# Performance work log

Hardware: AMD Instinct MI355X
Metric: run time of the kernel (lower is better)

## Reference

```python
import jax, jax.numpy as jnp
import numpy as np

H = 128

def _lstm_dir(x, w_ih, w_hh, b_ih, b_hh, reverse):
    # x: [B,T,D]; w_ih: [4H,D]; w_hh: [4H,H]; gate order i,f,g,o (PyTorch)
    B = x.shape[0]
    pre = jnp.einsum('btd,gd->btg', x, w_ih) + b_ih + b_hh  # [B,T,4H]
    if reverse:
        pre = pre[:, ::-1]
    pre = jnp.swapaxes(pre, 0, 1)  # [T,B,4H]
    h0 = jnp.zeros((B, H), dtype=x.dtype)
    c0 = jnp.zeros((B, H), dtype=x.dtype)

    def step(carry, xt):
        h, c = carry
        gates = xt + h @ w_hh.T
        i, f, g, o = jnp.split(gates, 4, axis=-1)
        c = jax.nn.sigmoid(f) * c + jax.nn.sigmoid(i) * jnp.tanh(g)
        h = jax.nn.sigmoid(o) * jnp.tanh(c)
        return (h, c), h

    _, hs = jax.lax.scan(step, (h0, c0), pre)  # hs: [T,B,H]
    hs = jnp.swapaxes(hs, 0, 1)  # [B,T,H]
    if reverse:
        hs = hs[:, ::-1]
    return hs

def _bilstm_layer(x, wf, rf):
    fwd = _lstm_dir(x, *wf, reverse=False)
    bwd = _lstm_dir(x, *rf, reverse=True)
    return jnp.concatenate([fwd, bwd], axis=-1)

def setup_inputs() -> dict:
    key = jax.random.key(0)
    ks = jax.random.split(key, 32)
    s = 0.05
    d = {'x': jax.random.normal(ks[0], (64, 512, 64), dtype=jnp.float32)}
    i = 1
    for l, din in [(0, 64), (1, 2 * H)]:
        for suf in ['', 'r']:
            d[f'w_ih_l{l}{suf}'] = s * jax.random.normal(ks[i], (4 * H, din)); i += 1
            d[f'w_hh_l{l}{suf}'] = s * jax.random.normal(ks[i], (4 * H, H)); i += 1
            d[f'b_ih_l{l}{suf}'] = s * jax.random.normal(ks[i], (4 * H,)); i += 1
            d[f'b_hh_l{l}{suf}'] = s * jax.random.normal(ks[i], (4 * H,)); i += 1
    d['w_fc'] = s * jax.random.normal(ks[i], (64, 2 * H)); i += 1
    d['b_fc'] = s * jax.random.normal(ks[i], (64,))
    return d

def reference(x, w_ih_l0, w_hh_l0, b_ih_l0, b_hh_l0, w_ih_l0r, w_hh_l0r, b_ih_l0r, b_hh_l0r, w_ih_l1, w_hh_l1, b_ih_l1, b_hh_l1, w_ih_l1r, w_hh_l1r, b_ih_l1r, b_hh_l1r, w_fc, b_fc):
    h = _bilstm_layer(x, (w_ih_l0, w_hh_l0, b_ih_l0, b_hh_l0), (w_ih_l0r, w_hh_l0r, b_ih_l0r, b_hh_l0r))
    h = _bilstm_layer(h, (w_ih_l1, w_hh_l1, b_ih_l1, b_hh_l1), (w_ih_l1r, w_hh_l1r, b_ih_l1r, b_hh_l1r))
    return h @ w_fc.T + b_fc
```

## Files before the change

### kernel.cpp

```cpp
#include <hip/hip_runtime.h>

#define TT 512
#define BB 64
#define HH 128
#define G4 512
#define PF 4

typedef float f32x4  __attribute__((ext_vector_type(4)));
typedef _Float16 f16x4v __attribute__((ext_vector_type(4)));
typedef _Float16 f16x8v __attribute__((ext_vector_type(8)));

__device__ __forceinline__ void barrier_lds_only() {
    asm volatile("s_waitcnt lgkmcnt(0)\n\ts_barrier" ::: "memory");
}

__global__ __launch_bounds__(256) void convert_f16(
    const float4* __restrict__ src, f16x4v* __restrict__ dst, int n4)
{
    for (int i = blockIdx.x * 256 + threadIdx.x; i < n4; i += gridDim.x * 256) {
        float4 f = src[i];
        f16x4v h;
        h[0] = (_Float16)f.x; h[1] = (_Float16)f.y;
        h[2] = (_Float16)f.z; h[3] = (_Float16)f.w;
        dst[i] = h;
    }
}

template<int K>
__global__ __launch_bounds__(256) void gemm_f16(
    const _Float16* __restrict__ Af, const _Float16* __restrict__ Wf,
    const float* __restrict__ b0, const float* __restrict__ b1,
    float* __restrict__ C)
{
    constexpr int NC  = K / 32;
    constexpr int LDA = 40;
    __shared__ _Float16 As[128 * LDA];
    __shared__ _Float16 Ws[128 * LDA];

    const int bm  = blockIdx.x * 128;
    const int bn  = blockIdx.y * 128;
    const int tid = threadIdx.x;
    const int wv  = tid >> 6;
    const int l   = tid & 63;
    const int jl  = l & 15;
    const int rg  = l >> 4;
    const int wr  = wv >> 1;
    const int wc  = wv & 1;

    const int sr = tid >> 1;
    const int sc = (tid & 1) * 16;

    const _Float16* Ap = Af + (size_t)(bm + sr) * K + sc;
    const _Float16* Wp = Wf + (size_t)(bn + sr) * K + sc;

    f32x4 acc[4][4];
    #pragma unroll
    for (int i = 0; i < 4; ++i)
        #pragma unroll
        for (int j = 0; j < 4; ++j)
            acc[i][j] = (f32x4){0.f, 0.f, 0.f, 0.f};

    f16x8v pa[2], pw[2];
    pa[0] = *(const f16x8v*)(Ap);     pa[1] = *(const f16x8v*)(Ap + 8);
    pw[0] = *(const f16x8v*)(Wp);     pw[1] = *(const f16x8v*)(Wp + 8);

    #pragma unroll 1
    for (int c = 0; c < NC; ++c) {
        __syncthreads();
        {
            int off = sr * LDA + sc;
            *(f16x8v*)&As[off]     = pa[0];
            *(f16x8v*)&As[off + 8] = pa[1];
            *(f16x8v*)&Ws[off]     = pw[0];
            *(f16x8v*)&Ws[off + 8] = pw[1];
        }
        __syncthreads();
        if (c + 1 < NC) {
            pa[0] = *(const f16x8v*)(Ap + (c + 1) * 32);
            pa[1] = *(const f16x8v*)(Ap + (c + 1) * 32 + 8);
            pw[0] = *(const f16x8v*)(Wp + (c + 1) * 32);
            pw[1] = *(const f16x8v*)(Wp + (c + 1) * 32 + 8);
        }
        f16x8v ah[4], wh[4];
        #pragma unroll
        for (int t = 0; t < 4; ++t) {
            ah[t] = *(const f16x8v*)&As[(wr * 64 + t * 16 + jl) * LDA + rg * 8];
            wh[t] = *(const f16x8v*)&Ws[(wc * 64 + t * 16 + jl) * LDA + rg * 8];
        }
        #pragma unroll
        for (int tm = 0; tm < 4; ++tm)
            #pragma unroll
            for (int tn = 0; tn < 4; ++tn)
                acc[tm][tn] = __builtin_amdgcn_mfma_f32_16x16x32_f16(
                    ah[tm], wh[tn], acc[tm][tn], 0, 0, 0);
    }

    #pragma unroll
    for (int tn = 0; tn < 4; ++tn) {
        int n = bn + wc * 64 + tn * 16 + jl;
        float bias = b0[n] + b1[n];
        #pragma unroll
        for (int tm = 0; tm < 4; ++tm) {
            int m = bm + wr * 64 + tm * 16 + rg * 4;
            #pragma unroll
            for (int r = 0; r < 4; ++r)
                C[(size_t)(m + r) * G4 + n] = acc[tm][tn][r] + bias;
        }
    }
}

__global__ __launch_bounds__(512) void lstm_scan_v14(
    const float* __restrict__ pre_f, const float* __restrict__ pre_b,
    const float* __restrict__ whh_f, const float* __restrict__ whh_b,
    float* __restrict__ out)
{
    const int dir = blockIdx.x >> 6;
    const int b   = blockIdx.x & 63;
    const float* __restrict__ pre  = dir ? pre_b : pre_f;
    const float* __restrict__ w_hh = dir ? whh_b : whh_f;

    const int tid = threadIdx.x;
    const int w   = tid >> 6;
    const int l   = tid & 63;
    const int jl  = l & 15;
    const int rg  = l >> 4;

    __shared__ _Float16 h_lds[2][HH];
    __shared__ float oring[2][PF][HH];

    f16x8v bw[4][4];
    #pragma unroll
    for (int cc = 0; cc < 4; ++cc) {
        const float* wr_ = w_hh + (size_t)(cc * HH + w * 16 + jl) * HH + rg * 8;
        #pragma unroll
        for (int kc = 0; kc < 4; ++kc) {
            const float* p_ = wr_ + kc * 32;
            f16x8v f;
            #pragma unroll
            for (int e = 0; e < 8; ++e) f[e] = (_Float16)p_[e];
            bw[cc][kc] = f;
        }
    }

    if (tid < 2 * HH) ((_Float16*)h_lds)[tid] = (_Float16)0.f;

    const size_t base = (size_t)b * TT * G4 + w * 16 + jl;
    float pf[PF][4];
    #pragma unroll
    for (int u = 0; u < PF; ++u) {
        int tau = dir ? (TT - 1 - u) : u;
        #pragma unroll
        for (int cc = 0; cc < 4; ++cc)
            pf[u][cc] = pre[base + (size_t)tau * G4 + cc * HH];
    }

    float c = 0.f;
    const float ASIG = -1.4426950408889634f;
    const float ATAN =  2.8853900817779268f;

    const int s_loc = tid >> 7;
    const int c128  = tid & 127;

    __syncthreads();

    for (int s0 = 0; s0 < TT; s0 += PF) {
        const int p = (s0 >> 2) & 1;
        #pragma unroll
        for (int u = 0; u < PF; ++u) {
            const int s = s0 + u;
            const int cur = u & 1;

            f16x8v a[4];
            #pragma unroll
            for (int kc = 0; kc < 4; ++kc)
                a[kc] = *(const f16x8v*)&h_lds[cur][kc * 32 + rg * 8];

            f32x4 acc[4];
            #pragma unroll
            for (int cc = 0; cc < 4; ++cc)
                acc[cc] = (f32x4){pf[u][cc], 0.f, 0.f, 0.f};

            {
                int sn = s + PF;
                int taun = dir ? (TT - 1 - sn) : sn;
                taun = taun < 0 ? 0 : (taun > TT - 1 ? TT - 1 : taun);
                #pragma unroll
                for (int cc = 0; cc < 4; ++cc)
                    pf[u][cc] = pre[base + (size_t)taun * G4 + cc * HH];
            }

            #pragma unroll
            for (int cc = 0; cc < 4; ++cc)
                #pragma unroll
                for (int kc = 0; kc < 4; ++kc)
                    acc[cc] = __builtin_amdgcn_mfma_f32_16x16x32_f16(
                        a[kc], bw[cc][kc], acc[cc], 0, 0, 0);

            if (l < 16) {
                float gi = acc[0][0], gf = acc[1][0], gg = acc[2][0], go = acc[3][0];
                float ei = __builtin_amdgcn_exp2f(ASIG * gi);
                float si = __builtin_amdgcn_rcpf(1.f + ei);
                float ef = __builtin_amdgcn_exp2f(ASIG * gf);
                float sf = __builtin_amdgcn_rcpf(1.f + ef);
                float eg = __builtin_amdgcn_exp2f(ATAN * gg);
                float tg = 1.f - 2.f * __builtin_amdgcn_rcpf(1.f + eg);
                float eo = __builtin_amdgcn_exp2f(ASIG * go);
                float so = __builtin_amdgcn_rcpf(1.f + eo);
                c = fmaf(sf, c, si * tg);
                float e2 = __builtin_amdgcn_exp2f(ATAN * c);
                float h  = so * (1.f - 2.f * __builtin_amdgcn_rcpf(1.f + e2));
                int j = w * 16 + l;
                h_lds[cur ^ 1][j] = (_Float16)h;
                oring[p][u][j] = h;
            }
            barrier_lds_only();
        }

        {
            int sb = s0 + s_loc;
            int tau = dir ? (TT - 1 - sb) : sb;
            out[((size_t)b * TT + tau) * (2 * HH) + dir * HH + c128] =
                oring[p][s_loc][c128];
        }
    }
}

__global__ __launch_bounds__(256) void fc_v2(
    const float* __restrict__ h2, const float* __restrict__ w_fc,
    const float* __restrict__ b_fc, float* __restrict__ out)
{
    __shared__ float4 wsT[64][64];
    const int tid = threadIdx.x;
    const int bm  = blockIdx.x * 64;
    const int n   = tid & 63;
    const int mg  = tid >> 6;

    #pragma unroll
    for (int qq = 0; qq < 16; ++qq) {
        int id = qq * 256 + tid;
        int nn = id >> 6, k4 = id & 63;
        wsT[k4][nn] = *(const float4*)&w_fc[(size_t)nn * 256 + k4 * 4];
    }
    __syncthreads();

    const float bias = b_fc[n];
    const float* hrow = h2 + (size_t)(bm + mg * 16) * 256;

    float acc[16];
    #pragma unroll
    for (int mi = 0; mi < 16; ++mi) acc[mi] = 0.f;

    #pragma unroll 2
    for (int k4 = 0; k4 < 64; ++k4) {
        float4 w4 = wsT[k4][n];
        #pragma unroll
        for (int mi = 0; mi < 16; ++mi) {
            float4 h4 = *(const float4*)(hrow + (size_t)mi * 256 + k4 * 4);
            acc[mi] = fmaf(h4.x, w4.x, acc[mi]);
            acc[mi] = fmaf(h4.y, w4.y, acc[mi]);
            acc[mi] = fmaf(h4.z, w4.z, acc[mi]);
            acc[mi] = fmaf(h4.w, w4.w, acc[mi]);
        }
    }
    #pragma unroll
    for (int mi = 0; mi < 16; ++mi)
        out[(size_t)(bm + mg * 16 + mi) * 64 + n] = acc[mi] + bias;
}

extern "C" void kernel_launch(void* const* d_in, const int* in_sizes, int n_in,
                              void* d_out, int out_size, void* d_ws, size_t ws_size,
                              hipStream_t stream) {
    const float* x        = (const float*)d_in[0];
    const float* w_ih_l0  = (const float*)d_in[1];
    const float* w_hh_l0  = (const float*)d_in[2];
    const float* b_ih_l0  = (const float*)d_in[3];
    const float* b_hh_l0  = (const float*)d_in[4];
    const float* w_ih_l0r = (const float*)d_in[5];
    const float* w_hh_l0r = (const float*)d_in[6];
    const float* b_ih_l0r = (const float*)d_in[7];
    const float* b_hh_l0r = (const float*)d_in[8];
    const float* w_ih_l1  = (const float*)d_in[9];
    const float* w_hh_l1  = (const float*)d_in[10];
    const float* b_ih_l1  = (const float*)d_in[11];
    const float* b_hh_l1  = (const float*)d_in[12];
    const float* w_ih_l1r = (const float*)d_in[13];
    const float* w_hh_l1r = (const float*)d_in[14];
    const float* b_ih_l1r = (const float*)d_in[15];
    const float* b_hh_l1r = (const float*)d_in[16];
    const float* w_fc     = (const float*)d_in[17];
    const float* b_fc     = (const float*)d_in[18];

    float* ws    = (float*)d_ws;
    float* pre_f = ws;
    float* pre_b = ws + 16777216;
    float* out0  = ws + 2 * 16777216;
    float* out1  = out0 + 8388608;

    _Float16* xf16  = (_Float16*)out0;
    _Float16* a1f16 = (_Float16*)out1;

    _Float16* wsp  = (_Float16*)d_out;
    _Float16* w0f  = wsp;
    _Float16* w0r  = wsp + 32768;
    _Float16* w1f  = wsp + 65536;
    _Float16* w1r  = wsp + 196608;

    dim3 gg(256, 4);

    convert_f16<<<32,   256, 0, stream>>>((const float4*)w_ih_l0,  (f16x4v*)w0f, 8192);
    convert_f16<<<32,   256, 0, stream>>>((const float4*)w_ih_l0r, (f16x4v*)w0r, 8192);
    convert_f16<<<128,  256, 0, stream>>>((const float4*)w_ih_l1,  (f16x4v*)w1f, 32768);
    convert_f16<<<128,  256, 0, stream>>>((const float4*)w_ih_l1r, (f16x4v*)w1r, 32768);

    convert_f16<<<2048, 256, 0, stream>>>((const float4*)x, (f16x4v*)xf16, 524288);
    gemm_f16<64><<<gg, 256, 0, stream>>>(xf16, w0f, b_ih_l0,  b_hh_l0,  pre_f);
    gemm_f16<64><<<gg, 256, 0, stream>>>(xf16, w0r, b_ih_l0r, b_hh_l0r, pre_b);
    lstm_scan_v14<<<128, 512, 0, stream>>>(pre_f, pre_b, w_hh_l0, w_hh_l0r, out0);

    convert_f16<<<2048, 256, 0, stream>>>((const float4*)out0, (f16x4v*)a1f16, 2097152);
    gemm_f16<256><<<gg, 256, 0, stream>>>(a1f16, w1f, b_ih_l1,  b_hh_l1,  pre_f);
    gemm_f16<256><<<gg, 256, 0, stream>>>(a1f16, w1r, b_ih_l1r, b_hh_l1r, pre_b);
    lstm_scan_v14<<<128, 512, 0, stream>>>(pre_f, pre_b, w_hh_l1, w_hh_l1r, out1);

    fc_v2<<<512, 256, 0, stream>>>(out1, w_fc, b_fc, (float*)d_out);
}
```

Baseline: 661.4 us.

## Store gate pre-activations and hidden outputs in fp16 across the pipeline

The input-projection GEMMs now write fp16 gate pre-activations. The LSTM scan reads them as fp16 and writes its hidden states directly as fp16, dropping the LDS staging ring and the separate conversion pass before the layer-1 GEMM. The FC kernel reads fp16 hidden states. This halves memory traffic for the intermediate buffers and removes one kernel, at the cost of reduced precision in pre-activations and outputs and uncoalesced per-step 2-byte stores from 16 lanes per wave.

```diff
diff --git a/kernel.cpp b/kernel.cpp
--- a/kernel.cpp
+++ b/kernel.cpp
@@ -30,7 +30,7 @@
 __global__ __launch_bounds__(256) void gemm_f16(
     const _Float16* __restrict__ Af, const _Float16* __restrict__ Wf,
     const float* __restrict__ b0, const float* __restrict__ b1,
-    float* __restrict__ C)
+    _Float16* __restrict__ C)
 {
     constexpr int NC  = K / 32;
     constexpr int LDA = 40;
@@ -104,20 +104,20 @@
             int m = bm + wr * 64 + tm * 16 + rg * 4;
             #pragma unroll
             for (int r = 0; r < 4; ++r)
-                C[(size_t)(m + r) * G4 + n] = acc[tm][tn][r] + bias;
-        }
-    }
-}
-
-__global__ __launch_bounds__(512) void lstm_scan_v14(
-    const float* __restrict__ pre_f, const float* __restrict__ pre_b,
+                C[(size_t)(m + r) * G4 + n] = (_Float16)(acc[tm][tn][r] + bias);
+        }
+    }
+}
+
+__global__ __launch_bounds__(512) void lstm_scan_v15(
+    const _Float16* __restrict__ pre_f, const _Float16* __restrict__ pre_b,
     const float* __restrict__ whh_f, const float* __restrict__ whh_b,
-    float* __restrict__ out)
+    _Float16* __restrict__ out)
 {
     const int dir = blockIdx.x >> 6;
     const int b   = blockIdx.x & 63;
-    const float* __restrict__ pre  = dir ? pre_b : pre_f;
-    const float* __restrict__ w_hh = dir ? whh_b : whh_f;
+    const _Float16* __restrict__ pre = dir ? pre_b : pre_f;
+    const float* __restrict__ w_hh   = dir ? whh_b : whh_f;
 
     const int tid = threadIdx.x;
     const int w   = tid >> 6;
@@ -126,7 +126,6 @@
     const int rg  = l >> 4;
 
     __shared__ _Float16 h_lds[2][HH];
-    __shared__ float oring[2][PF][HH];
 
     f16x8v bw[4][4];
     #pragma unroll
@@ -151,20 +150,16 @@
         int tau = dir ? (TT - 1 - u) : u;
         #pragma unroll
         for (int cc = 0; cc < 4; ++cc)
-            pf[u][cc] = pre[base + (size_t)tau * G4 + cc * HH];
+            pf[u][cc] = (float)pre[base + (size_t)tau * G4 + cc * HH];
     }
 
     float c = 0.f;
     const float ASIG = -1.4426950408889634f;
     const float ATAN =  2.8853900817779268f;
 
-    const int s_loc = tid >> 7;
-    const int c128  = tid & 127;
-
     __syncthreads();
 
     for (int s0 = 0; s0 < TT; s0 += PF) {
-        const int p = (s0 >> 2) & 1;
         #pragma unroll
         for (int u = 0; u < PF; ++u) {
             const int s = s0 + u;
@@ -186,7 +181,7 @@
                 taun = taun < 0 ? 0 : (taun > TT - 1 ? TT - 1 : taun);
                 #pragma unroll
                 for (int cc = 0; cc < 4; ++cc)
-                    pf[u][cc] = pre[base + (size_t)taun * G4 + cc * HH];
+                    pf[u][cc] = (float)pre[base + (size_t)taun * G4 + cc * HH];
             }
 
             #pragma unroll
@@ -208,25 +203,20 @@
                 float so = __builtin_amdgcn_rcpf(1.f + eo);
                 c = fmaf(sf, c, si * tg);
                 float e2 = __builtin_amdgcn_exp2f(ATAN * c);
-                float h  = so * (1.f - 2.f * __builtin_amdgcn_rcpf(1.f + e2));
+                float hval = so * (1.f - 2.f * __builtin_amdgcn_rcpf(1.f + e2));
                 int j = w * 16 + l;
-                h_lds[cur ^ 1][j] = (_Float16)h;
-                oring[p][u][j] = h;
+                _Float16 h16 = (_Float16)hval;
+                h_lds[cur ^ 1][j] = h16;
+                int tau = dir ? (TT - 1 - s) : s;
+                out[((size_t)b * TT + tau) * (2 * HH) + dir * HH + j] = h16;
             }
             barrier_lds_only();
         }
-
-        {
-            int sb = s0 + s_loc;
-            int tau = dir ? (TT - 1 - sb) : sb;
-            out[((size_t)b * TT + tau) * (2 * HH) + dir * HH + c128] =
-                oring[p][s_loc][c128];
-        }
-    }
-}
-
-__global__ __launch_bounds__(256) void fc_v2(
-    const float* __restrict__ h2, const float* __restrict__ w_fc,
+    }
+}
+
+__global__ __launch_bounds__(256) void fc_v3(
+    const _Float16* __restrict__ h2, const float* __restrict__ w_fc,
     const float* __restrict__ b_fc, float* __restrict__ out)
 {
     __shared__ float4 wsT[64][64];
@@ -244,7 +234,7 @@
     __syncthreads();
 
     const float bias = b_fc[n];
-    const float* hrow = h2 + (size_t)(bm + mg * 16) * 256;
+    const _Float16* hrow = h2 + (size_t)(bm + mg * 16) * 256;
 
     float acc[16];
     #pragma unroll
@@ -255,11 +245,11 @@
         float4 w4 = wsT[k4][n];
         #pragma unroll
         for (int mi = 0; mi < 16; ++mi) {
-            float4 h4 = *(const float4*)(hrow + (size_t)mi * 256 + k4 * 4);
-            acc[mi] = fmaf(h4.x, w4.x, acc[mi]);
-            acc[mi] = fmaf(h4.y, w4.y, acc[mi]);
-            acc[mi] = fmaf(h4.z, w4.z, acc[mi]);
-            acc[mi] = fmaf(h4.w, w4.w, acc[mi]);
+            f16x4v hv = *(const f16x4v*)(hrow + (size_t)mi * 256 + k4 * 4);
+            acc[mi] = fmaf((float)hv[0], w4.x, acc[mi]);
+            acc[mi] = fmaf((float)hv[1], w4.y, acc[mi]);
+            acc[mi] = fmaf((float)hv[2], w4.z, acc[mi]);
+            acc[mi] = fmaf((float)hv[3], w4.w, acc[mi]);
         }
     }
     #pragma unroll
@@ -290,20 +280,16 @@
     const float* w_fc     = (const float*)d_in[17];
     const float* b_fc     = (const float*)d_in[18];
 
-    float* ws    = (float*)d_ws;
-    float* pre_f = ws;
-    float* pre_b = ws + 16777216;
-    float* out0  = ws + 2 * 16777216;
-    float* out1  = out0 + 8388608;
-
-    _Float16* xf16  = (_Float16*)out0;
-    _Float16* a1f16 = (_Float16*)out1;
-
-    _Float16* wsp  = (_Float16*)d_out;
-    _Float16* w0f  = wsp;
-    _Float16* w0r  = wsp + 32768;
-    _Float16* w1f  = wsp + 65536;
-    _Float16* w1r  = wsp + 196608;
+    _Float16* wsh    = (_Float16*)d_ws;
+    _Float16* preh_f = wsh;
+    _Float16* preh_b = preh_f + 16777216;
+    _Float16* out0h  = preh_b + 16777216;
+    _Float16* out1h  = out0h  + 8388608;
+    _Float16* xf16   = out1h  + 8388608;
+    _Float16* w0f    = xf16   + 2097152;
+    _Float16* w0r    = w0f    + 32768;
+    _Float16* w1f    = w0r    + 32768;
+    _Float16* w1r    = w1f    + 131072;
 
     dim3 gg(256, 4);
 
@@ -311,16 +297,15 @@
     convert_f16<<<32,   256, 0, stream>>>((const float4*)w_ih_l0r, (f16x4v*)w0r, 8192);
     convert_f16<<<128,  256, 0, stream>>>((const float4*)w_ih_l1,  (f16x4v*)w1f, 32768);
     convert_f16<<<128,  256, 0, stream>>>((const float4*)w_ih_l1r, (f16x4v*)w1r, 32768);
-
     convert_f16<<<2048, 256, 0, stream>>>((const float4*)x, (f16x4v*)xf16, 524288);
-    gemm_f16<64><<<gg, 256, 0, stream>>>(xf16, w0f, b_ih_l0,  b_hh_l0,  pre_f);
-    gemm_f16<64><<<gg, 256, 0, stream>>>(xf16, w0r, b_ih_l0r, b_hh_l0r, pre_b);
-    lstm_scan_v14<<<128, 512, 0, stream>>>(pre_f, pre_b, w_hh_l0, w_hh_l0r, out0);
-
-    convert_f16<<<2048, 256, 0, stream>>>((const float4*)out0, (f16x4v*)a1f16, 2097152);
-    gemm_f16<256><<<gg, 256, 0, stream>>>(a1f16, w1f, b_ih_l1,  b_hh_l1,  pre_f);
-    gemm_f16<256><<<gg, 256, 0, stream>>>(a1f16, w1r, b_ih_l1r, b_hh_l1r, pre_b);
-    lstm_scan_v14<<<128, 512, 0, stream>>>(pre_f, pre_b, w_hh_l1, w_hh_l1r, out1);
-
-    fc_v2<<<512, 256, 0, stream>>>(out1, w_fc, b_fc, (float*)d_out);
-}
+
+    gemm_f16<64><<<gg, 256, 0, stream>>>(xf16, w0f, b_ih_l0,  b_hh_l0,  preh_f);
+    gemm_f16<64><<<gg, 256, 0, stream>>>(xf16, w0r, b_ih_l0r, b_hh_l0r, preh_b);
+    lstm_scan_v15<<<128, 512, 0, stream>>>(preh_f, preh_b, w_hh_l0, w_hh_l0r, out0h);
+
+    gemm_f16<256><<<gg, 256, 0, stream>>>(out0h, w1f, b_ih_l1,  b_hh_l1,  preh_f);
+    gemm_f16<256><<<gg, 256, 0, stream>>>(out0h, w1r, b_ih_l1r, b_hh_l1r, preh_b);
+    lstm_scan_v15<<<128, 512, 0, stream>>>(preh_f, preh_b, w_hh_l1, w_hh_l1r, out1h);
+
+    fc_v3<<<512, 256, 0, stream>>>(out1h, w_fc, b_fc, (float*)d_out);
+}
```

Result: faster. 571.9 us (-13.5%).
